# Kernel optimization log

Hardware: AMD Instinct MI355X
Metric: run time of the kernel (lower is better)

The kernel has to match this reference:

```python
import jax, jax.numpy as jnp
import numpy as np

jax.config.update("jax_enable_x64", True)

NUM_OF_LSB_TO_IGNORE = 5
COMPARISON_NUM_BITS_IGNORED = 5
SCALE = 65536.0  # activations live on an integer-share-like scale so bit shifts matter

BLOCK_SIZES = np.array([[0, 1]] * 32 + [[2, 2]] * 48 + [[4, 4]] * 48)
# active (non-identity) block sizes and the channel indices they own
ACTIVE = [(tuple(int(v) for v in bs), np.where(np.all(BLOCK_SIZES == bs, axis=1))[0])
          for bs in np.unique(BLOCK_SIZES, axis=0) if 0 not in bs]


def setup_inputs() -> dict:
    key = jax.random.key(0)
    activation = jax.random.normal(key, (16, 128, 114, 114), dtype=jnp.float32) * SCALE
    return {"activation": activation}


def _block_sign(x, bh, bw):
    # x: [N, c, H, W]. Pad bottom/right to block multiples, space-to-depth,
    # integer floor-mean per block, LSB truncation via int16 wrap, sign >= 0.
    N, c, H, W = x.shape
    ph, pw = (-H) % bh, (-W) % bw
    xp = jnp.pad(x, ((0, 0), (0, 0), (0, ph), (0, pw)))
    xr = xp.reshape(N, c, (H + ph) // bh, bh, (W + pw) // bw, bw)
    s = xr.sum(axis=(3, 5)).astype(jnp.int64)          # block sums
    mean = s // (bh * bw)                               # integer floor mean
    q = ((mean >> NUM_OF_LSB_TO_IGNORE).astype(jnp.int16)
         .astype(jnp.int64)) << COMPARISON_NUM_BITS_IGNORED
    sign = q >= 0                                       # DReLU
    # broadcast block sign back to pixels, then unpad
    sign = jnp.repeat(jnp.repeat(sign, bh, axis=2), bw, axis=3)
    return sign[:, :, :H, :W]


def reference(activation):
    out = activation
    for (bh, bw), ch in ACTIVE:  # small fixed set of block-size groups
        cur = activation[:, ch]
        sign = _block_sign(cur, bh, bw)
        out = out.at[:, ch].set(cur * sign.astype(activation.dtype))
    return out
```

## Files before the change

### kernel.cpp

```cpp
#include <hip/hip_runtime.h>


typedef float v4 __attribute__((ext_vector_type(4)));

#define PLANE 12996
#define NBLK_A 6498
#define NBLK_B 7680
#define NBLK_C 7680

__global__ __launch_bounds__(256) void sbrelu_strip(const float* __restrict__ in,
                                                    float* __restrict__ out) {
    __shared__ v4 Ls[342];
    __shared__ float Lm[342];
    const int bid = blockIdx.x;
    const int tid = threadIdx.x;

    if (bid < NBLK_A) {
        int idx = bid * 256 + tid;
        int n = idx / 103968;
        int off = n * 415872 + (idx - n * 103968);
        ((v4*)out)[off] = ((const v4*)in)[off];
        return;
    }

    int u, cls;
    if (bid < NBLK_A + NBLK_B) { u = bid - NBLK_A; cls = 0; }
    else                       { u = bid - NBLK_A - NBLK_B; cls = 1; }
    const int p  = u / 10;
    const int r  = u - 10 * p;
    const int n  = p / 48;
    const int cr = p - n * 48;
    const int c  = cls ? (80 + cr) : (32 + cr);
    const int nrows = (r < 9) ? 12 : 6;
    const int nf4 = (nrows * 114) >> 2;

    const v4* __restrict__ ip = (const v4*)(in  + (size_t)(n * 128 + c) * PLANE + 12 * r * 114);
    v4* __restrict__       op = (v4*)(out + (size_t)(n * 128 + c) * PLANE + 12 * r * 114);

    for (int i = tid; i < nf4; i += 256) Ls[i] = ip[i];
    __syncthreads();

    const float* Lf = (const float*)Ls;
    if (cls == 0) {
        int ncell = (nrows >> 1) * 57;
        for (int m = tid; m < ncell; m += 256) {
            int br = m / 57;
            int cw = m - 57 * br;
            const float* q0 = Lf + 228 * br + 2 * cw;
            float s = ((q0[0] + q0[1]) + q0[114]) + q0[115];
            Lm[m] = (s > -1.0f) ? 1.0f : 0.0f;
        }
    } else {
        int ncell = ((r < 9) ? 3 : 2) * 29;
        for (int m = tid; m < ncell; m += 256) {
            int br = m / 29;
            int cw = m - 29 * br;
            int nh = (3 * r + br == 28) ? 2 : 4;
            int nw = (cw == 28) ? 2 : 4;
            const float* q0 = Lf + 456 * br + 4 * cw;
            float s = 0.0f;
            for (int k = 0; k < nh; ++k)
                for (int j = 0; j < nw; ++j) s += q0[114 * k + j];
            Lm[m] = (s > -1.0f) ? 1.0f : 0.0f;
        }
    }
    __syncthreads();

    if (cls == 0) {
        for (int i = tid; i < nf4; i += 256) {
            v4 v = Ls[i];
            int q = 4 * i;
            int hl = q / 114;
            int w  = q - 114 * hl;
            v4 o;
#pragma unroll
            for (int e = 0; e < 4; ++e) {
                o[e] = v[e] * Lm[(hl >> 1) * 57 + (w >> 1)];
                if (++w == 114) { w = 0; ++hl; }
            }
            op[i] = o;
        }
    } else {
        for (int i = tid; i < nf4; i += 256) {
            v4 v = Ls[i];
            int q = 4 * i;
            int hl = q / 114;
            int w  = q - 114 * hl;
            v4 o;
#pragma unroll
            for (int e = 0; e < 4; ++e) {
                o[e] = v[e] * Lm[(hl >> 2) * 29 + (w >> 2)];
                if (++w == 114) { w = 0; ++hl; }
            }
            op[i] = o;
        }
    }
}

extern "C" void kernel_launch(void* const* d_in, const int* in_sizes, int n_in,
                              void* d_out, int out_size, void* d_ws, size_t ws_size,
                              hipStream_t stream) {
    const float* in = (const float*)d_in[0];
    float* out = (float*)d_out;
    sbrelu_strip<<<NBLK_A + NBLK_B + NBLK_C, 256, 0, stream>>>(in, out);
}
```

Before: 187.5 us.

## Replace LDS strip staging with per-wave register block processing

Instead of staging 12-row strips into shared memory with two barriers, each wavefront now handles one block-row directly: lanes load their block's float2 pixels into registers, compute the block sign, and write scaled outputs. This removes LDS traffic and __syncthreads and raises block count granularity. In exchange, global accesses become float2-sized with strided per-lane patterns (stride 2 float2 for 4x4 blocks), and some lanes idle (57 or 29 of 64 active), which may hurt coalescing.

Result: no change. 187.2 us (median of 2 runs) (-0.2%).

```diff
diff --git a/kernel.cpp b/kernel.cpp
--- a/kernel.cpp
+++ b/kernel.cpp
@@ -3,15 +3,15 @@
 
 typedef float v4 __attribute__((ext_vector_type(4)));
 
-#define PLANE 12996
+#define PLANE  12996
 #define NBLK_A 6498
-#define NBLK_B 7680
-#define NBLK_C 7680
+#define NU_B   43776
+#define NBLK_B 10944
+#define NU_C   22272
+#define NBLK_C 5568
 
-__global__ __launch_bounds__(256) void sbrelu_strip(const float* __restrict__ in,
-                                                    float* __restrict__ out) {
-    __shared__ v4 Ls[342];
-    __shared__ float Lm[342];
+__global__ __launch_bounds__(256) void sbrelu_reg(const float* __restrict__ in,
+                                                  float* __restrict__ out) {
     const int bid = blockIdx.x;
     const int tid = threadIdx.x;
 
@@ -23,76 +23,73 @@
         return;
     }
 
-    int u, cls;
-    if (bid < NBLK_A + NBLK_B) { u = bid - NBLK_A; cls = 0; }
-    else                       { u = bid - NBLK_A - NBLK_B; cls = 1; }
-    const int p  = u / 10;
-    const int r  = u - 10 * p;
-    const int n  = p / 48;
-    const int cr = p - n * 48;
-    const int c  = cls ? (80 + cr) : (32 + cr);
-    const int nrows = (r < 9) ? 12 : 6;
-    const int nf4 = (nrows * 114) >> 2;
+    const int lane = tid & 63;
+    const int wid  = tid >> 6;
 
-    const v4* __restrict__ ip = (const v4*)(in  + (size_t)(n * 128 + c) * PLANE + 12 * r * 114);
-    v4* __restrict__       op = (v4*)(out + (size_t)(n * 128 + c) * PLANE + 12 * r * 114);
+    if (bid < NBLK_A + NBLK_B) {
+        int u  = (bid - NBLK_A) * 4 + wid;
+        int p  = u / 57;
+        int rp = u - 57 * p;
+        int n  = p / 48;
+        int c  = 32 + (p - 48 * n);
+        size_t base = (size_t)(n * 128 + c) * PLANE + 228 * rp;
+        if (lane < 57) {
+            const float2* i0 = (const float2*)(in + base) + lane;
+            float2 a = i0[0];
+            float2 b = i0[57];
+            float s = ((a.x + a.y) + b.x) + b.y;
+            float m = (s > -1.0f) ? 1.0f : 0.0f;
+            float2* o0 = (float2*)(out + base) + lane;
+            o0[0]  = make_float2(a.x * m, a.y * m);
+            o0[57] = make_float2(b.x * m, b.y * m);
+        }
+        return;
+    }
 
-    for (int i = tid; i < nf4; i += 256) Ls[i] = ip[i];
-    __syncthreads();
+    int u  = (bid - NBLK_A - NBLK_B) * 4 + wid;
+    int p  = u / 29;
+    int br = u - 29 * p;
+    int n  = p / 48;
+    int c  = 80 + (p - 48 * n);
+    size_t base = (size_t)(n * 128 + c) * PLANE + 456 * br;
+    if (lane >= 29) return;
+    const bool full = (lane != 28);
+    const float2* q  = (const float2*)(in  + base) + 2 * lane;
+    float2*       qo = (float2*)      (out + base) + 2 * lane;
 
-    const float* Lf = (const float*)Ls;
-    if (cls == 0) {
-        int ncell = (nrows >> 1) * 57;
-        for (int m = tid; m < ncell; m += 256) {
-            int br = m / 57;
-            int cw = m - 57 * br;
-            const float* q0 = Lf + 228 * br + 2 * cw;
-            float s = ((q0[0] + q0[1]) + q0[114]) + q0[115];
-            Lm[m] = (s > -1.0f) ? 1.0f : 0.0f;
+    if (br != 28) {
+        float2 a0 = q[0],  a1 = q[57],  a2 = q[114], a3 = q[171];
+        float2 b0 = make_float2(0.f, 0.f), b1 = b0, b2 = b0, b3 = b0;
+        if (full) { b0 = q[1]; b1 = q[58]; b2 = q[115]; b3 = q[172]; }
+        float s = 0.0f;
+        s += a0.x; s += a0.y; if (full) { s += b0.x; s += b0.y; }
+        s += a1.x; s += a1.y; if (full) { s += b1.x; s += b1.y; }
+        s += a2.x; s += a2.y; if (full) { s += b2.x; s += b2.y; }
+        s += a3.x; s += a3.y; if (full) { s += b3.x; s += b3.y; }
+        float m = (s > -1.0f) ? 1.0f : 0.0f;
+        qo[0]   = make_float2(a0.x * m, a0.y * m);
+        qo[57]  = make_float2(a1.x * m, a1.y * m);
+        qo[114] = make_float2(a2.x * m, a2.y * m);
+        qo[171] = make_float2(a3.x * m, a3.y * m);
+        if (full) {
+            qo[1]   = make_float2(b0.x * m, b0.y * m);
+            qo[58]  = make_float2(b1.x * m, b1.y * m);
+            qo[115] = make_float2(b2.x * m, b2.y * m);
+            qo[172] = make_float2(b3.x * m, b3.y * m);
         }
     } else {
-        int ncell = ((r < 9) ? 3 : 2) * 29;
-        for (int m = tid; m < ncell; m += 256) {
-            int br = m / 29;
-            int cw = m - 29 * br;
-            int nh = (3 * r + br == 28) ? 2 : 4;
-            int nw = (cw == 28) ? 2 : 4;
-            const float* q0 = Lf + 456 * br + 4 * cw;
-            float s = 0.0f;
-            for (int k = 0; k < nh; ++k)
-                for (int j = 0; j < nw; ++j) s += q0[114 * k + j];
-            Lm[m] = (s > -1.0f) ? 1.0f : 0.0f;
-        }
-    }
-    __syncthreads();
-
-    if (cls == 0) {
-        for (int i = tid; i < nf4; i += 256) {
-            v4 v = Ls[i];
-            int q = 4 * i;
-            int hl = q / 114;
-            int w  = q - 114 * hl;
-            v4 o;
-#pragma unroll
-            for (int e = 0; e < 4; ++e) {
-                o[e] = v[e] * Lm[(hl >> 1) * 57 + (w >> 1)];
-                if (++w == 114) { w = 0; ++hl; }
-            }
-            op[i] = o;
-        }
-    } else {
-        for (int i = tid; i < nf4; i += 256) {
-            v4 v = Ls[i];
-            int q = 4 * i;
-            int hl = q / 114;
-            int w  = q - 114 * hl;
-            v4 o;
-#pragma unroll
-            for (int e = 0; e < 4; ++e) {
-                o[e] = v[e] * Lm[(hl >> 2) * 29 + (w >> 2)];
-                if (++w == 114) { w = 0; ++hl; }
-            }
-            op[i] = o;
+        float2 a0 = q[0], a1 = q[57];
+        float2 b0 = make_float2(0.f, 0.f), b1 = b0;
+        if (full) { b0 = q[1]; b1 = q[58]; }
+        float s = 0.0f;
+        s += a0.x; s += a0.y; if (full) { s += b0.x; s += b0.y; }
+        s += a1.x; s += a1.y; if (full) { s += b1.x; s += b1.y; }
+        float m = (s > -1.0f) ? 1.0f : 0.0f;
+        qo[0]  = make_float2(a0.x * m, a0.y * m);
+        qo[57] = make_float2(a1.x * m, a1.y * m);
+        if (full) {
+            qo[1]  = make_float2(b0.x * m, b0.y * m);
+            qo[58] = make_float2(b1.x * m, b1.y * m);
         }
     }
 }
@@ -102,5 +99,5 @@
                               hipStream_t stream) {
     const float* in = (const float*)d_in[0];
     float* out = (float*)d_out;
-    sbrelu_strip<<<NBLK_A + NBLK_B + NBLK_C, 256, 0, stream>>>(in, out);
+    sbrelu_reg<<<NBLK_A + NBLK_B + NBLK_C, 256, 0, stream>>>(in, out);
 }
```

## Split into three kernels and compute block signs with wave shuffles

Applied to the files above, without the earlier changes.

The single fused strip kernel, which staged rows in LDS, is replaced by three launches. One is a grid-stride copy for identity channels. The other two assign one wavefront per 2-row or 4-row strip and form block sums with cross-lane shuffles instead of shared memory and __syncthreads. This removes the LDS round trips, the barriers and the index division per element. In exchange there are three kernel launches instead of one, some lanes sit idle (57 of 64 active), and the shuffle lane mapping is intricate and easy to get wrong.

Measured after the change: 189.4 us. Within noise of the previous version (+1.0%).

```diff
diff --git a/kernel.cpp b/kernel.cpp
--- a/kernel.cpp
+++ b/kernel.cpp
@@ -3,96 +3,132 @@
 
 typedef float v4 __attribute__((ext_vector_type(4)));
 
-#define PLANE 12996
-#define NBLK_A 6498
-#define NBLK_B 7680
-#define NBLK_C 7680
+#define PLANE     12996
+#define NA4       1663488
+#define A_PER_N   103968
+#define A_NSTRIDE 415872
+#define NU_B      43776
+#define NU_C      22272
 
-__global__ __launch_bounds__(256) void sbrelu_strip(const float* __restrict__ in,
-                                                    float* __restrict__ out) {
-    __shared__ v4 Ls[342];
-    __shared__ float Lm[342];
-    const int bid = blockIdx.x;
-    const int tid = threadIdx.x;
+__global__ __launch_bounds__(256) void sbrelu_a(const float* __restrict__ in,
+                                                float* __restrict__ out) {
+    const v4* __restrict__ vin = (const v4*)in;
+    v4* __restrict__ vout = (v4*)out;
+    int t = blockIdx.x * 256 + threadIdx.x;
+    int S = gridDim.x * 256;
+    for (int i = t; i < NA4; i += S) {
+        int n = i / A_PER_N;
+        int o = n * A_NSTRIDE + (i - n * A_PER_N);
+        vout[o] = vin[o];
+    }
+}
 
-    if (bid < NBLK_A) {
-        int idx = bid * 256 + tid;
-        int n = idx / 103968;
-        int off = n * 415872 + (idx - n * 103968);
-        ((v4*)out)[off] = ((const v4*)in)[off];
-        return;
+__global__ __launch_bounds__(256) void sbrelu_b(const float* __restrict__ in,
+                                                float* __restrict__ out) {
+    const int lane = threadIdx.x & 63;
+    const int u = blockIdx.x * 4 + (threadIdx.x >> 6);
+    const int p = u / 57;
+    const int rp = u - 57 * p;
+    const int n = p / 48;
+    const int c = 32 + (p - 48 * n);
+    const size_t base = (size_t)(n * 128 + c) * PLANE + 228 * rp;
+    const v4* __restrict__ ip = (const v4*)(in + base);
+    v4* __restrict__ op = (v4*)(out + base);
+
+    const int ll = (lane < 57) ? lane : 56;
+    v4 v = ip[ll];
+
+    float z28 = __shfl(v.z, (lane + 28) & 63);
+    float w28 = __shfl(v.w, (lane + 28) & 63);
+    float x29 = __shfl(v.x, (lane + 29) & 63);
+    float y29 = __shfl(v.y, (lane + 29) & 63);
+
+    float se = ((v.x + v.y) + z28) + w28;
+    float so = ((v.z + v.w) + x29) + y29;
+    float pe = (se > -1.0f) ? 1.0f : 0.0f;
+    float po = (so > -1.0f) ? 1.0f : 0.0f;
+
+    float f_pe = __shfl(pe, (lane <= 28) ? lane : 0);
+    float f_po = __shfl(po, (lane >= 29) ? lane - 29 : 0);
+    float g_po = __shfl(po, (lane <= 27) ? lane : 0);
+    float g_pe = __shfl(pe, (lane == 28) ? 0 : ((lane >= 29) ? lane - 28 : 0));
+    float mf = (lane <= 28) ? f_pe : f_po;
+    float ms = (lane <= 27) ? g_po : g_pe;
+
+    if (lane < 57) {
+        v4 o;
+        o.x = v.x * mf; o.y = v.y * mf;
+        o.z = v.z * ms; o.w = v.w * ms;
+        op[ll] = o;
+    }
+}
+
+__global__ __launch_bounds__(256) void sbrelu_c(const float* __restrict__ in,
+                                                float* __restrict__ out) {
+    const int lane = threadIdx.x & 63;
+    const int u = blockIdx.x * 4 + (threadIdx.x >> 6);
+    const int p = u / 29;
+    const int ch = u - 29 * p;
+    const int n = p / 48;
+    const int c = 80 + (p - 48 * n);
+    const size_t base = (size_t)(n * 128 + c) * PLANE + 456 * ch;
+    const v4* __restrict__ ip = (const v4*)(in + base);
+    v4* __restrict__ op = (v4*)(out + base);
+    const int ll = (lane < 57) ? lane : 56;
+    const int s1 = (lane + 28) & 63;
+    const int s2 = (lane + 29) & 63;
+    const bool fullc = (ch != 28);
+
+    v4 v, w;
+    float msk;
+    if (fullc) {
+        v = ip[ll];
+        w = ip[57 + ll];
+        float az = __shfl(v.z, s1), aw = __shfl(v.w, s1);
+        float bz = __shfl(w.z, s1), bw = __shfl(w.w, s1);
+        float cx = __shfl(v.x, s2), cy = __shfl(v.y, s2);
+        float dx = __shfl(w.x, s2), dy = __shfl(w.y, s2);
+        float s = 0.0f;
+        if (lane != 28) {
+            s += v.x; s += v.y; s += v.z; s += v.w;
+            s += az;  s += aw;  s += cx;  s += cy;
+            s += w.x; s += w.y; s += w.z; s += w.w;
+            s += bz;  s += bw;  s += dx;  s += dy;
+        } else {
+            s += v.x; s += v.y;
+            s += az;  s += aw;
+            s += w.x; s += w.y;
+            s += bz;  s += bw;
+        }
+        msk = (s > -1.0f) ? 1.0f : 0.0f;
+    } else {
+        v = ip[ll];
+        float az = __shfl(v.z, s1), aw = __shfl(v.w, s1);
+        float cx = __shfl(v.x, s2), cy = __shfl(v.y, s2);
+        float s = 0.0f;
+        if (lane != 28) {
+            s += v.x; s += v.y; s += v.z; s += v.w;
+            s += az;  s += aw;  s += cx;  s += cy;
+        } else {
+            s += v.x; s += v.y;
+            s += az;  s += aw;
+        }
+        msk = (s > -1.0f) ? 1.0f : 0.0f;
     }
 
-    int u, cls;
-    if (bid < NBLK_A + NBLK_B) { u = bid - NBLK_A; cls = 0; }
-    else                       { u = bid - NBLK_A - NBLK_B; cls = 1; }
-    const int p  = u / 10;
-    const int r  = u - 10 * p;
-    const int n  = p / 48;
-    const int cr = p - n * 48;
-    const int c  = cls ? (80 + cr) : (32 + cr);
-    const int nrows = (r < 9) ? 12 : 6;
-    const int nf4 = (nrows * 114) >> 2;
+    float mf = __shfl(msk, (lane <= 28) ? lane : lane - 29);
+    float ms = __shfl(msk, (lane <= 27) ? lane : ((lane == 28) ? 0 : lane - 28));
 
-    const v4* __restrict__ ip = (const v4*)(in  + (size_t)(n * 128 + c) * PLANE + 12 * r * 114);
-    v4* __restrict__       op = (v4*)(out + (size_t)(n * 128 + c) * PLANE + 12 * r * 114);
-
-    for (int i = tid; i < nf4; i += 256) Ls[i] = ip[i];
-    __syncthreads();
-
-    const float* Lf = (const float*)Ls;
-    if (cls == 0) {
-        int ncell = (nrows >> 1) * 57;
-        for (int m = tid; m < ncell; m += 256) {
-            int br = m / 57;
-            int cw = m - 57 * br;
-            const float* q0 = Lf + 228 * br + 2 * cw;
-            float s = ((q0[0] + q0[1]) + q0[114]) + q0[115];
-            Lm[m] = (s > -1.0f) ? 1.0f : 0.0f;
-        }
-    } else {
-        int ncell = ((r < 9) ? 3 : 2) * 29;
-        for (int m = tid; m < ncell; m += 256) {
-            int br = m / 29;
-            int cw = m - 29 * br;
-            int nh = (3 * r + br == 28) ? 2 : 4;
-            int nw = (cw == 28) ? 2 : 4;
-            const float* q0 = Lf + 456 * br + 4 * cw;
-            float s = 0.0f;
-            for (int k = 0; k < nh; ++k)
-                for (int j = 0; j < nw; ++j) s += q0[114 * k + j];
-            Lm[m] = (s > -1.0f) ? 1.0f : 0.0f;
-        }
-    }
-    __syncthreads();
-
-    if (cls == 0) {
-        for (int i = tid; i < nf4; i += 256) {
-            v4 v = Ls[i];
-            int q = 4 * i;
-            int hl = q / 114;
-            int w  = q - 114 * hl;
-            v4 o;
-#pragma unroll
-            for (int e = 0; e < 4; ++e) {
-                o[e] = v[e] * Lm[(hl >> 1) * 57 + (w >> 1)];
-                if (++w == 114) { w = 0; ++hl; }
-            }
-            op[i] = o;
-        }
-    } else {
-        for (int i = tid; i < nf4; i += 256) {
-            v4 v = Ls[i];
-            int q = 4 * i;
-            int hl = q / 114;
-            int w  = q - 114 * hl;
-            v4 o;
-#pragma unroll
-            for (int e = 0; e < 4; ++e) {
-                o[e] = v[e] * Lm[(hl >> 2) * 29 + (w >> 2)];
-                if (++w == 114) { w = 0; ++hl; }
-            }
-            op[i] = o;
+    if (lane < 57) {
+        v4 o;
+        o.x = v.x * mf; o.y = v.y * mf;
+        o.z = v.z * ms; o.w = v.w * ms;
+        op[ll] = o;
+        if (fullc) {
+            v4 o2;
+            o2.x = w.x * mf; o2.y = w.y * mf;
+            o2.z = w.z * ms; o2.w = w.w * ms;
+            op[57 + ll] = o2;
         }
     }
 }
@@ -102,5 +138,7 @@
                               hipStream_t stream) {
     const float* in = (const float*)d_in[0];
     float* out = (float*)d_out;
-    sbrelu_strip<<<NBLK_A + NBLK_B + NBLK_C, 256, 0, stream>>>(in, out);
+    sbrelu_a<<<2048, 256, 0, stream>>>(in, out);
+    sbrelu_b<<<NU_B / 4, 256, 0, stream>>>(in, out);
+    sbrelu_c<<<NU_C / 4, 256, 0, stream>>>(in, out);
 }
```
